# Optimization experiments

Measured on AMD Instinct MI355X. Metric: run time of the kernel, lower is better.

Reference implementation:

```python
import jax, jax.numpy as jnp
import numpy as np

B, N, K = 4, 8192, 16
EMBED, HID, NCLS = 64, 128, 13
EPS = 1e-5


def _bn(x, g, b):
    # BatchNorm1d in training mode: stats over all points (B*N), per channel
    m = jnp.mean(x, axis=(0, 1), keepdims=True)
    v = jnp.var(x, axis=(0, 1), keepdims=True)
    return (x - m) * jax.lax.rsqrt(v + EPS) * g + b


def _knn_idx(pos, k):
    # pos: [B,N,3] -> k nearest neighbor indices per point (self excluded)
    sq = jnp.sum(pos * pos, -1)  # [B,N]
    d2 = sq[:, :, None] + sq[:, None, :] - 2.0 * jnp.einsum('bnd,bmd->bnm', pos, pos)
    n = pos.shape[1]
    d2 = d2 + jnp.eye(n, dtype=pos.dtype) * 1e10  # mask self (loop=False)
    _, idx = jax.lax.top_k(-d2, k)  # [B,N,k]
    return idx


def _pt_conv(x, pos, idx, w_lin, w_src, w_dst, pos_w, pos_b):
    # PyG PointTransformerConv: vector attention over neighbors (incl. self loop)
    Bc = x.shape[0]
    bidx = jnp.arange(Bc)[:, None, None]
    v = x @ w_lin          # value:  lin(x)
    a_src = x @ w_src      # lin_src(x)
    a_dst = x @ w_dst      # lin_dst(x)
    vj = v[bidx, idx]                      # [B,N,k1,C]
    aj = a_src[bidx, idx]                  # [B,N,k1,C]
    pj = pos[bidx, idx]                    # [B,N,k1,3]
    delta = (pos[:, :, None, :] - pj) @ pos_w + pos_b   # pos_nn(pos_i - pos_j)
    attn = jax.nn.softmax(a_dst[:, :, None, :] - aj + delta, axis=2)
    return jnp.sum(attn * (vj + delta), axis=2)  # sum aggregation


def setup_inputs() -> dict:
    key = jax.random.key(0)
    ks = jax.random.split(key, 20)

    def w(k, fan_in, fan_out):
        return (jax.random.normal(k, (fan_in, fan_out), jnp.float32) / np.sqrt(fan_in)).astype(jnp.float32)

    inp = {
        'points': jax.random.normal(ks[0], (B, N, 3), jnp.float32),
        'embed_w1': w(ks[1], 3, EMBED), 'embed_b1': jnp.zeros((EMBED,), jnp.float32),
        'bn1_g': jnp.ones((EMBED,), jnp.float32), 'bn1_b': jnp.zeros((EMBED,), jnp.float32),
        'embed_w2': w(ks[2], EMBED, EMBED), 'embed_b2': jnp.zeros((EMBED,), jnp.float32),
        'bne_g': jnp.ones((EMBED,), jnp.float32), 'bne_b': jnp.zeros((EMBED,), jnp.float32),
        'l0_lin': w(ks[3], EMBED, HID), 'l0_src': w(ks[4], EMBED, HID), 'l0_dst': w(ks[5], EMBED, HID),
        'l0_pos_w': w(ks[6], 3, HID), 'l0_pos_b': jnp.zeros((HID,), jnp.float32),
        'l0_bn_g': jnp.ones((HID,), jnp.float32), 'l0_bn_b': jnp.zeros((HID,), jnp.float32),
        'l1_lin': w(ks[7], HID, HID), 'l1_src': w(ks[8], HID, HID), 'l1_dst': w(ks[9], HID, HID),
        'l1_pos_w': w(ks[10], 3, HID), 'l1_pos_b': jnp.zeros((HID,), jnp.float32),
        'l1_bn_g': jnp.ones((HID,), jnp.float32), 'l1_bn_b': jnp.zeros((HID,), jnp.float32),
        'dec_w1': w(ks[11], HID, HID), 'dec_b1': jnp.zeros((HID,), jnp.float32),
        'dec_bn_g': jnp.ones((HID,), jnp.float32), 'dec_bn_b': jnp.zeros((HID,), jnp.float32),
        'dec_w2': w(ks[12], HID, NCLS), 'dec_b2': jnp.zeros((NCLS,), jnp.float32),
    }
    return inp


def reference(points, embed_w1, embed_b1, bn1_g, bn1_b, embed_w2, embed_b2,
              bne_g, bne_b,
              l0_lin, l0_src, l0_dst, l0_pos_w, l0_pos_b, l0_bn_g, l0_bn_b,
              l1_lin, l1_src, l1_dst, l1_pos_w, l1_pos_b, l1_bn_g, l1_bn_b,
              dec_w1, dec_b1, dec_bn_g, dec_bn_b, dec_w2, dec_b2):
    Bc, Nc, _ = points.shape
    # embedding MLP: Linear -> BN -> ReLU -> Linear, then BN -> ReLU
    h = points @ embed_w1 + embed_b1
    h = jax.nn.relu(_bn(h, bn1_g, bn1_b))
    h = h @ embed_w2 + embed_b2
    x = jax.nn.relu(_bn(h, bne_g, bne_b))
    # kNN graph (per batch), then append self loop (add_self_loops=True)
    idx = _knn_idx(points, K)
    self_idx = jnp.broadcast_to(jnp.arange(Nc)[None, :, None], (Bc, Nc, 1))
    idxf = jnp.concatenate([idx, self_idx], axis=-1)  # [B,N,K+1]
    x = jax.nn.relu(_bn(_pt_conv(x, points, idxf, l0_lin, l0_src, l0_dst, l0_pos_w, l0_pos_b), l0_bn_g, l0_bn_b))
    x = jax.nn.relu(_bn(_pt_conv(x, points, idxf, l1_lin, l1_src, l1_dst, l1_pos_w, l1_pos_b), l1_bn_g, l1_bn_b))
    # decoder MLP (dropout = identity at inference)
    h = jax.nn.relu(_bn(x @ dec_w1 + dec_b1, dec_bn_g, dec_bn_b))
    logits = h @ dec_w2 + dec_b2  # [B,N,num_classes]
    return logits
```

## Files before the change

### kernel.cpp

```cpp
#include <hip/hip_runtime.h>
#include <math.h>

#define BB 4
#define NN 8192
#define PP 32768
#define KNN 16
#define KINF 3.4e38f
#define PADIDX 0x7fffffff

typedef float f32x2 __attribute__((ext_vector_type(2)));
typedef float f32x4 __attribute__((ext_vector_type(4)));

__device__ __forceinline__ f32x2 pk_mul(f32x2 a, f32x2 b) {
  f32x2 d; asm("v_pk_mul_f32 %0, %1, %2" : "=v"(d) : "v"(a), "v"(b)); return d;
}
__device__ __forceinline__ f32x2 pk_add(f32x2 a, f32x2 b) {
  f32x2 d; asm("v_pk_add_f32 %0, %1, %2" : "=v"(d) : "v"(a), "v"(b)); return d;
}

__global__ __launch_bounds__(256) void k_embed1(const float* __restrict__ pts,
    const float* __restrict__ w1, const float* __restrict__ b1, float* __restrict__ h1)
{
  int tid = threadIdx.x;
  int c = tid & 63, g = tid >> 6;
  float wx = w1[c], wy = w1[64 + c], wz = w1[128 + c], bc = b1[c];
  int base = blockIdx.x * 256;
  #pragma unroll 4
  for (int i = 0; i < 64; ++i) {
    int p = base + g + i * 4;
    float px = pts[p*3+0], py = pts[p*3+1], pz = pts[p*3+2];
    float h = fmaf(pz, wz, fmaf(py, wy, fmaf(px, wx, bc)));
    h1[(size_t)p*64 + c] = h;
  }
}

__global__ __launch_bounds__(256) void k_prep(const float* __restrict__ pts, float* __restrict__ pp)
{
  int t = blockIdx.x * 256 + threadIdx.x;
  int b = t >> 12, m = t & 4095;
  int c = m >> 4, l = m & 15;
  int jl = b * NN + c * 32 + l;
  int jh = jl + 16;
  float xl = pts[jl*3+0], yl = pts[jl*3+1], zl = pts[jl*3+2];
  float xh = pts[jh*3+0], yh = pts[jh*3+1], zh = pts[jh*3+2];
  float wl = __fadd_rn(__fadd_rn(__fmul_rn(xl,xl), __fmul_rn(yl,yl)), __fmul_rn(zl,zl));
  float wh = __fadd_rn(__fadd_rn(__fmul_rn(xh,xh), __fmul_rn(yh,yh)), __fmul_rn(zh,zh));
  float* o = pp + (size_t)t * 8;
  *(float4*)(o + 0) = make_float4(xl, xh, yl, yh);
  *(float4*)(o + 4) = make_float4(zl, zh, wl, wh);
}

template<int C>
__global__ __launch_bounds__(256) void k_stats(const float* __restrict__ src,
    float* __restrict__ gsum, float* __restrict__ gss)
{
  constexpr int GPB = 256 / C;
  int tid = threadIdx.x;
  int c = tid % C, g = tid / C;
  float s = 0.f, ss = 0.f;
  for (int p = blockIdx.x * GPB + g; p < PP; p += gridDim.x * GPB) {
    float v = src[(size_t)p*C + c];
    s += v; ss = fmaf(v, v, ss);
  }
  __shared__ float ls[256], lq[256];
  ls[tid] = s; lq[tid] = ss;
  __syncthreads();
  if (tid < C) {
    float a = 0.f, b2 = 0.f;
    #pragma unroll
    for (int i = 0; i < GPB; ++i) { a += ls[tid + i*C]; b2 += lq[tid + i*C]; }
    atomicAdd(gsum + tid, a);
    atomicAdd(gss + tid, b2);
  }
}

__global__ void k_finalize(int C, const float* __restrict__ gsum, const float* __restrict__ gss,
    const float* __restrict__ gg, const float* __restrict__ bb,
    float* __restrict__ sc, float* __restrict__ sh)
{
  int c = threadIdx.x;
  if (c >= C) return;
  float mean = gsum[c] * (1.0f / PP);
  float var  = gss[c] * (1.0f / PP) - mean * mean;
  float s = gg[c] / sqrtf(var + 1e-5f);
  sc[c] = s;
  sh[c] = bb[c] - mean * s;
}

template<int K, int COUT>
__global__ __launch_bounds__(256) void k_proj(const float* __restrict__ in,
    const float* __restrict__ sc, const float* __restrict__ sh,
    const float* __restrict__ W0, const float* __restrict__ W1, const float* __restrict__ W2,
    const float* __restrict__ B0, const float* __restrict__ B1, const float* __restrict__ B2,
    float* __restrict__ O0, float* __restrict__ O1, float* __restrict__ O2)
{
  constexpr int PTS = 64;
  constexpr int CW = 8;
  constexpr int CG = COUT / CW;
  constexpr int PW = PTS * CG / 256;
  const float* W  = (blockIdx.y == 0) ? W0 : (blockIdx.y == 1) ? W1 : W2;
  const float* Bb = (blockIdx.y == 0) ? B0 : (blockIdx.y == 1) ? B1 : B2;
  float*       O  = (blockIdx.y == 0) ? O0 : (blockIdx.y == 1) ? O1 : O2;
  __shared__ float xs[PTS][K + 1];
  int tid = threadIdx.x;
  int pbase = blockIdx.x * PTS;
  constexpr int T4 = PTS * K / 4;
  for (int i = tid; i < T4; i += 256) {
    int p = i / (K/4), k = (i % (K/4)) * 4;
    float4 v = *(const float4*)(in + (size_t)(pbase + p)*K + k);
    v.x = fmaxf(fmaf(v.x, sc[k+0], sh[k+0]), 0.f);
    v.y = fmaxf(fmaf(v.y, sc[k+1], sh[k+1]), 0.f);
    v.z = fmaxf(fmaf(v.z, sc[k+2], sh[k+2]), 0.f);
    v.w = fmaxf(fmaf(v.w, sc[k+3], sh[k+3]), 0.f);
    xs[p][k+0] = v.x; xs[p][k+1] = v.y; xs[p][k+2] = v.z; xs[p][k+3] = v.w;
  }
  __syncthreads();
  int cg = tid % CG, pg = tid / CG;
  int c0 = cg * CW, p0 = pg * PW;
  float acc[PW][CW];
  #pragma unroll
  for (int i = 0; i < PW; ++i) {
    #pragma unroll
    for (int j = 0; j < CW; ++j) acc[i][j] = 0.f;
  }
  #pragma unroll 4
  for (int k = 0; k < K; ++k) {
    float4 wa = *(const float4*)(W + (size_t)k*COUT + c0);
    float4 wb = *(const float4*)(W + (size_t)k*COUT + c0 + 4);
    #pragma unroll
    for (int i = 0; i < PW; ++i) {
      float x = xs[p0 + i][k];
      acc[i][0] = fmaf(x, wa.x, acc[i][0]);
      acc[i][1] = fmaf(x, wa.y, acc[i][1]);
      acc[i][2] = fmaf(x, wa.z, acc[i][2]);
      acc[i][3] = fmaf(x, wa.w, acc[i][3]);
      acc[i][4] = fmaf(x, wb.x, acc[i][4]);
      acc[i][5] = fmaf(x, wb.y, acc[i][5]);
      acc[i][6] = fmaf(x, wb.z, acc[i][6]);
      acc[i][7] = fmaf(x, wb.w, acc[i][7]);
    }
  }
  float bj[CW];
  #pragma unroll
  for (int j = 0; j < CW; ++j) bj[j] = Bb ? Bb[c0 + j] : 0.f;
  #pragma unroll
  for (int i = 0; i < PW; ++i) {
    float* op = O + (size_t)(pbase + p0 + i)*COUT + c0;
    *(float4*)(op)     = make_float4(acc[i][0]+bj[0], acc[i][1]+bj[1], acc[i][2]+bj[2], acc[i][3]+bj[3]);
    *(float4*)(op + 4) = make_float4(acc[i][4]+bj[4], acc[i][5]+bj[5], acc[i][6]+bj[6], acc[i][7]+bj[7]);
  }
}

__global__ __launch_bounds__(256, 8) void k_knn(const float* __restrict__ pp, int* __restrict__ idxout)
{
  __shared__ uint2 buf[256];
  int tid = threadIdx.x;
  int lane = tid & 63;
  int l16 = lane & 15;
  int g64 = lane & 48;
  uint2* wbuf = buf + (tid >> 6) * 64;
  int wv = (blockIdx.x * 256 + tid) >> 6;
  int b  = wv >> 11;
  int qbase = (wv * 4) & (NN - 1);
  int qc = qbase >> 5;
  int qr = (qbase & 31) + (lane >> 4);
  const float* pb = pp + (size_t)b * (NN * 4);

  float qx, qy, qz, qw;
  {
    int qslot = qc * 16 + (qr & 15);
    int qh = (qr >> 4) & 1;
    const float* qp = pb + (size_t)qslot * 8 + qh;
    qx = qp[0]; qy = qp[2]; qz = qp[4]; qw = qp[6];
  }
  f32x2 qx2; qx2.x = qx; qx2.y = qx;
  f32x2 qy2; qy2.x = qy; qy2.y = qy;
  f32x2 qz2; qz2.x = qz; qz2.y = qz;
  f32x2 qw2; qw2.x = qw; qw2.y = qw;

  float lval = KINF; int lidx = PADIDX;
  float pval = KINF; int pidx = PADIDX;
  int   pcnt = 0;
  float tau  = KINF;
  unsigned lmask = (1u << l16) - 1;

  auto flush = [&]() {
    float v = (l16 >= pcnt) ? KINF : pval;
    int  ix = (l16 >= pcnt) ? PADIDX : pidx;
    #pragma unroll
    for (int k = 2; k <= 16; k <<= 1) {
      #pragma unroll
      for (int m = k >> 1; m >= 1; m >>= 1) {
        float ov = __shfl_xor(v, m, 16);
        int   oi = __shfl_xor(ix, m, 16);
        bool dirUp = (l16 & k) == 0;
        bool lower = (l16 & m) == 0;
        bool oLt = (ov < v) || (ov == v && oi < ix);
        if ((dirUp == lower) ? oLt : !oLt) { v = ov; ix = oi; }
      }
    }
    float rv = __shfl_xor(v, 15, 16);
    int   ri = __shfl_xor(ix, 15, 16);
    bool t = (rv < lval) || (rv == lval && ri < lidx);
    float nv = t ? rv : lval;
    int   ni = t ? ri : lidx;
    #pragma unroll
    for (int m = 8; m >= 1; m >>= 1) {
      float ov = __shfl_xor(nv, m, 16);
      int   oi = __shfl_xor(ni, m, 16);
      bool lower = (l16 & m) == 0;
      bool oLt = (ov < nv) || (ov == nv && oi < ni);
      if (lower ? oLt : !oLt) { nv = ov; ni = oi; }
    }
    lval = nv; lidx = ni;
    tau = __shfl(lval, 15, 16);
    pcnt = 0;
  };

  auto append = [&](unsigned long long bal, bool hit, float d2, int j) {
    unsigned slice = (unsigned)(bal >> g64) & 0xffffu;
    int h   = __popc(slice);
    int pos = __popc(slice & lmask);
    if (__ballot(pcnt + h > 16)) flush();
    if (hit) wbuf[g64 + pcnt + pos] = make_uint2(__float_as_uint(d2), (unsigned)j);
    uint2 r = wbuf[lane];
    bool targ = (l16 >= pcnt) && (l16 < pcnt + h);
    pval = targ ? __uint_as_float(r.x) : pval;
    pidx = targ ? (int)r.y : pidx;
    pcnt += h;
  };

  const float* cp = pb + (size_t)l16 * 8;
  for (int c = 0; c < 256; ++c) {
    f32x4 A  = *(const f32x4*)(cp + 0);
    f32x4 Bq = *(const f32x4*)(cp + 4);
    cp += 128;
    f32x2 xs = __builtin_shufflevector(A, A, 0, 1);
    f32x2 ys = __builtin_shufflevector(A, A, 2, 3);
    f32x2 zs = __builtin_shufflevector(Bq, Bq, 0, 1);
    f32x2 ws = __builtin_shufflevector(Bq, Bq, 2, 3);
    f32x2 dot = pk_add(pk_add(pk_mul(qx2, xs), pk_mul(qy2, ys)), pk_mul(qz2, zs));
    f32x2 s2  = pk_add(qw2, ws);
    f32x2 t2  = pk_add(dot, dot);
    float d2lo = __fsub_rn(s2.x, t2.x);
    float d2hi = __fsub_rn(s2.y, t2.y);
    if (c == qc) {
      bool lo = qr < 16;
      int  tl = lo ? qr : qr - 16;
      if (l16 == tl) { if (lo) d2lo = KINF; else d2hi = KINF; }
    }
    bool hlo = d2lo < tau;
    unsigned long long blo = __ballot(hlo);
    if (blo) append(blo, hlo, d2lo, c * 32 + l16);
    bool hhi = d2hi < tau;
    unsigned long long bhi = __ballot(hhi);
    if (bhi) append(bhi, hhi, d2hi, c * 32 + 16 + l16);
  }
  flush();

  idxout[(size_t)wv * 64 + lane] = lidx;
}

__global__ __launch_bounds__(256) void k_conv(const float* __restrict__ V, const float* __restrict__ S,
    const float* __restrict__ D, const float* __restrict__ pts, const int* __restrict__ idx,
    const float* __restrict__ pw, const float* __restrict__ pbv, float* __restrict__ Y)
{
  int lane = threadIdx.x & 63;
  int wid  = (blockIdx.x * 256 + threadIdx.x) >> 6;
  int c0 = lane * 2;
  float2 w0  = *(const float2*)(pw + c0);
  float2 w1  = *(const float2*)(pw + 128 + c0);
  float2 w2  = *(const float2*)(pw + 256 + c0);
  float2 pb2 = *(const float2*)(pbv + c0);
  for (int p = wid; p < PP; p += 4096) {
    int b = p >> 13, self = p & (NN - 1);
    const float* pbase = pts + (size_t)b * NN * 3;
    float pix = pbase[self*3+0], piy = pbase[self*3+1], piz = pbase[self*3+2];
    float2 di = *(const float2*)(D + (size_t)p*128 + c0);
    float m0 = -3.4e38f, m1 = -3.4e38f, l0 = 0.f, l1 = 0.f, a0 = 0.f, a1 = 0.f;
    for (int t = 0; t < 17; ++t) {
      int j = (t < 16) ? idx[p*KNN + t] : self;
      float dx = pix - pbase[j*3+0];
      float dy = piy - pbase[j*3+1];
      float dz = piz - pbase[j*3+2];
      size_t off = ((size_t)b * NN + j) * 128 + c0;
      float2 sj = *(const float2*)(S + off);
      float2 vj = *(const float2*)(V + off);
      float de0 = fmaf(dz, w2.x, fmaf(dy, w1.x, fmaf(dx, w0.x, pb2.x)));
      float de1 = fmaf(dz, w2.y, fmaf(dy, w1.y, fmaf(dx, w0.y, pb2.y)));
      float g0 = di.x - sj.x + de0;
      float g1 = di.y - sj.y + de1;
      float mn0 = fmaxf(m0, g0), mn1 = fmaxf(m1, g1);
      float cr0 = __expf(m0 - mn0), cr1 = __expf(m1 - mn1);
      float e0  = __expf(g0 - mn0), e1  = __expf(g1 - mn1);
      l0 = fmaf(l0, cr0, e0);
      l1 = fmaf(l1, cr1, e1);
      a0 = fmaf(a0, cr0, e0 * (vj.x + de0));
      a1 = fmaf(a1, cr1, e1 * (vj.y + de1));
      m0 = mn0; m1 = mn1;
    }
    float2 o; o.x = a0 / l0; o.y = a1 / l1;
    *(float2*)(Y + (size_t)p*128 + c0) = o;
  }
}

__global__ __launch_bounds__(256) void k_dec2(const float* __restrict__ T,
    const float* __restrict__ sc, const float* __restrict__ sh,
    const float* __restrict__ W, const float* __restrict__ bias, float* __restrict__ out)
{
  __shared__ float xs[64][132];
  __shared__ float wt[13][128];
  int tid = threadIdx.x;
  int pb = blockIdx.x * 64;
  for (int i = tid; i < 13 * 128; i += 256) {
    int cls = i >> 7, k = i & 127;
    wt[cls][k] = W[k*13 + cls];
  }
  for (int i = tid; i < 64 * 32; i += 256) {
    int p = i >> 5, k = (i & 31) * 4;
    float4 v = *(const float4*)(T + (size_t)(pb + p)*128 + k);
    v.x = fmaxf(fmaf(v.x, sc[k+0], sh[k+0]), 0.f);
    v.y = fmaxf(fmaf(v.y, sc[k+1], sh[k+1]), 0.f);
    v.z = fmaxf(fmaf(v.z, sc[k+2], sh[k+2]), 0.f);
    v.w = fmaxf(fmaf(v.w, sc[k+3], sh[k+3]), 0.f);
    xs[p][k+0] = v.x; xs[p][k+1] = v.y; xs[p][k+2] = v.z; xs[p][k+3] = v.w;
  }
  __syncthreads();
  for (int o = tid; o < 64 * 13; o += 256) {
    int p = o / 13, cls = o - p * 13;
    float acc = bias[cls];
    const float4* xr = (const float4*)&xs[p][0];
    const float4* wr = (const float4*)&wt[cls][0];
    #pragma unroll 8
    for (int k4 = 0; k4 < 32; ++k4) {
      float4 a = xr[k4], w = wr[k4];
      acc = fmaf(a.x, w.x, acc);
      acc = fmaf(a.y, w.y, acc);
      acc = fmaf(a.z, w.z, acc);
      acc = fmaf(a.w, w.w, acc);
    }
    out[(size_t)(pb + p)*13 + cls] = acc;
  }
}

extern "C" void kernel_launch(void* const* d_in, const int* in_sizes, int n_in,
                              void* d_out, int out_size, void* d_ws, size_t ws_size,
                              hipStream_t stream)
{
  const float* pts      = (const float*)d_in[0];
  const float* embed_w1 = (const float*)d_in[1];
  const float* embed_b1 = (const float*)d_in[2];
  const float* bn1_g    = (const float*)d_in[3];
  const float* bn1_b    = (const float*)d_in[4];
  const float* embed_w2 = (const float*)d_in[5];
  const float* embed_b2 = (const float*)d_in[6];
  const float* bne_g    = (const float*)d_in[7];
  const float* bne_b    = (const float*)d_in[8];
  const float* l0_lin   = (const float*)d_in[9];
  const float* l0_src   = (const float*)d_in[10];
  const float* l0_dst   = (const float*)d_in[11];
  const float* l0_pos_w = (const float*)d_in[12];
  const float* l0_pos_b = (const float*)d_in[13];
  const float* l0_bn_g  = (const float*)d_in[14];
  const float* l0_bn_b  = (const float*)d_in[15];
  const float* l1_lin   = (const float*)d_in[16];
  const float* l1_src   = (const float*)d_in[17];
  const float* l1_dst   = (const float*)d_in[18];
  const float* l1_pos_w = (const float*)d_in[19];
  const float* l1_pos_b = (const float*)d_in[20];
  const float* l1_bn_g  = (const float*)d_in[21];
  const float* l1_bn_b  = (const float*)d_in[22];
  const float* dec_w1   = (const float*)d_in[23];
  const float* dec_b1   = (const float*)d_in[24];
  const float* dec_bn_g = (const float*)d_in[25];
  const float* dec_bn_b = (const float*)d_in[26];
  const float* dec_w2   = (const float*)d_in[27];
  const float* dec_b2   = (const float*)d_in[28];

  char* ws = (char*)d_ws;
  const size_t MB = 1024 * 1024;
  float* h1  = (float*)(ws + 0);
  float* h2  = (float*)(ws + 8*MB);
  int*   idx = (int*)  (ws + 16*MB);
  float* v0  = (float*)(ws + 18*MB);
  float* s0  = (float*)(ws + 34*MB);
  float* d0  = (float*)(ws + 50*MB);
  float* y0  = (float*)(ws + 66*MB);
  float* y1  = (float*)(ws + 82*MB);
  float* tt  = (float*)(ws + 0);
  float* pairs8 = (float*)(ws + 18*MB);
  float* st  = (float*)(ws + 98*MB);
  float *sum1=st+0,    *ss1=st+64,   *sc1=st+128,  *sh1=st+192;
  float *sum2=st+256,  *ss2=st+320,  *sc2=st+384,  *sh2=st+448;
  float *sum3=st+512,  *ss3=st+640,  *sc3=st+768,  *sh3=st+896;
  float *sum4=st+1024, *ss4=st+1152, *sc4=st+1280, *sh4=st+1408;
  float *sum5=st+1536, *ss5=st+1664, *sc5=st+1792, *sh5=st+1920;

  hipMemsetAsync(st, 0, 2048 * sizeof(float), stream);

  k_prep<<<64, 256, 0, stream>>>(pts, pairs8);
  k_knn<<<2048, 256, 0, stream>>>(pairs8, idx);

  k_embed1<<<128, 256, 0, stream>>>(pts, embed_w1, embed_b1, h1);
  k_stats<64><<<512, 256, 0, stream>>>(h1, sum1, ss1);
  k_finalize<<<1, 64, 0, stream>>>(64, sum1, ss1, bn1_g, bn1_b, sc1, sh1);
  k_proj<64,64><<<dim3(512,1), 256, 0, stream>>>(h1, sc1, sh1,
      embed_w2, embed_w2, embed_w2, embed_b2, embed_b2, embed_b2, h2, h2, h2);
  k_stats<64><<<512, 256, 0, stream>>>(h2, sum2, ss2);
  k_finalize<<<1, 64, 0, stream>>>(64, sum2, ss2, bne_g, bne_b, sc2, sh2);

  k_proj<64,128><<<dim3(512,3), 256, 0, stream>>>(h2, sc2, sh2,
      l0_lin, l0_src, l0_dst, nullptr, nullptr, nullptr, v0, s0, d0);
  k_conv<<<1024, 256, 0, stream>>>(v0, s0, d0, pts, idx, l0_pos_w, l0_pos_b, y0);
  k_stats<128><<<512, 256, 0, stream>>>(y0, sum3, ss3);
  k_finalize<<<1, 128, 0, stream>>>(128, sum3, ss3, l0_bn_g, l0_bn_b, sc3, sh3);

  k_proj<128,128><<<dim3(512,3), 256, 0, stream>>>(y0, sc3, sh3,
      l1_lin, l1_src, l1_dst, nullptr, nullptr, nullptr, v0, s0, d0);
  k_conv<<<1024, 256, 0, stream>>>(v0, s0, d0, pts, idx, l1_pos_w, l1_pos_b, y1);
  k_stats<128><<<512, 256, 0, stream>>>(y1, sum4, ss4);
  k_finalize<<<1, 128, 0, stream>>>(128, sum4, ss4, l1_bn_g, l1_bn_b, sc4, sh4);

  k_proj<128,128><<<dim3(512,1), 256, 0, stream>>>(y1, sc4, sh4,
      dec_w1, dec_w1, dec_w1, dec_b1, dec_b1, dec_b1, tt, tt, tt);
  k_stats<128><<<512, 256, 0, stream>>>(tt, sum5, ss5);
  k_finalize<<<1, 128, 0, stream>>>(128, sum5, ss5, dec_bn_g, dec_bn_b, sc5, sh5);
  k_dec2<<<512, 256, 0, stream>>>(tt, sc5, sh5, dec_w2, dec_b2, (float*)d_out);
}
```

Baseline: 698.9 us.

## Process four query groups per wave in kNN to reuse candidate loads

Each wave in the kNN kernel now handles 16 queries (4 register-blocked groups of 4) instead of 4, so every candidate point loaded from memory is compared against four times as many queries. Candidate loads are software-prefetched one iteration ahead. The pending-buffer handling is simplified: flush now reads directly from LDS instead of maintaining a register copy on every append. The grid shrinks to 512 blocks and the occupancy hint is removed, trading parallelism and occupancy for higher register use and more per-wave work.

New measurement: 802.0 us. 1.15x slower.

```diff
diff --git a/kernel.cpp b/kernel.cpp
--- a/kernel.cpp
+++ b/kernel.cpp
@@ -151,42 +151,43 @@
   }
 }
 
-__global__ __launch_bounds__(256, 8) void k_knn(const float* __restrict__ pp, int* __restrict__ idxout)
-{
-  __shared__ uint2 buf[256];
+__global__ __launch_bounds__(256) void k_knn(const float* __restrict__ pp, int* __restrict__ idxout)
+{
+  __shared__ uint2 buf[4][4][64];
   int tid = threadIdx.x;
   int lane = tid & 63;
   int l16 = lane & 15;
+  int g   = lane >> 4;
   int g64 = lane & 48;
-  uint2* wbuf = buf + (tid >> 6) * 64;
-  int wv = (blockIdx.x * 256 + tid) >> 6;
-  int b  = wv >> 11;
-  int qbase = (wv * 4) & (NN - 1);
-  int qc = qbase >> 5;
-  int qr = (qbase & 31) + (lane >> 4);
+  int wid = tid >> 6;
+  int wv = blockIdx.x * 4 + wid;
+  int b  = wv >> 9;
+  int qbase = (wv & 511) << 4;
+  int qc    = qbase >> 5;
+  int qhalf = (qbase >> 4) & 1;
   const float* pb = pp + (size_t)b * (NN * 4);
 
-  float qx, qy, qz, qw;
-  {
-    int qslot = qc * 16 + (qr & 15);
-    int qh = (qr >> 4) & 1;
-    const float* qp = pb + (size_t)qslot * 8 + qh;
-    qx = qp[0]; qy = qp[2]; qz = qp[4]; qw = qp[6];
-  }
-  f32x2 qx2; qx2.x = qx; qx2.y = qx;
-  f32x2 qy2; qy2.x = qy; qy2.y = qy;
-  f32x2 qz2; qz2.x = qz; qz2.y = qz;
-  f32x2 qw2; qw2.x = qw; qw2.y = qw;
-
-  float lval = KINF; int lidx = PADIDX;
-  float pval = KINF; int pidx = PADIDX;
-  int   pcnt = 0;
-  float tau  = KINF;
+  f32x2 qx2[4], qy2[4], qz2[4], qw2[4];
+  #pragma unroll
+  for (int r = 0; r < 4; ++r) {
+    const float* qp = pb + (size_t)(qc * 16 + r * 4 + g) * 8 + qhalf;
+    float x = qp[0], y = qp[2], z = qp[4], w = qp[6];
+    qx2[r].x = x; qx2[r].y = x;
+    qy2[r].x = y; qy2[r].y = y;
+    qz2[r].x = z; qz2[r].y = z;
+    qw2[r].x = w; qw2[r].y = w;
+  }
+
+  float lval[4]; int lidx[4]; float tau[4]; int pcnt[4];
+  #pragma unroll
+  for (int r = 0; r < 4; ++r) { lval[r] = KINF; lidx[r] = PADIDX; tau[r] = KINF; pcnt[r] = 0; }
   unsigned lmask = (1u << l16) - 1;
-
-  auto flush = [&]() {
-    float v = (l16 >= pcnt) ? KINF : pval;
-    int  ix = (l16 >= pcnt) ? PADIDX : pidx;
+  int sdiff = l16 - g;
+
+  auto flush = [&](int r) {
+    uint2 e = buf[wid][r][lane];
+    float v  = (l16 < pcnt[r]) ? __uint_as_float(e.x) : KINF;
+    int  ix  = (l16 < pcnt[r]) ? (int)e.y : PADIDX;
     #pragma unroll
     for (int k = 2; k <= 16; k <<= 1) {
       #pragma unroll
@@ -201,9 +202,9 @@
     }
     float rv = __shfl_xor(v, 15, 16);
     int   ri = __shfl_xor(ix, 15, 16);
-    bool t = (rv < lval) || (rv == lval && ri < lidx);
-    float nv = t ? rv : lval;
-    int   ni = t ? ri : lidx;
+    bool t = (rv < lval[r]) || (rv == lval[r] && ri < lidx[r]);
+    float nv = t ? rv : lval[r];
+    int   ni = t ? ri : lidx[r];
     #pragma unroll
     for (int m = 8; m >= 1; m >>= 1) {
       float ov = __shfl_xor(nv, m, 16);
@@ -212,53 +213,59 @@
       bool oLt = (ov < nv) || (ov == nv && oi < ni);
       if (lower ? oLt : !oLt) { nv = ov; ni = oi; }
     }
-    lval = nv; lidx = ni;
-    tau = __shfl(lval, 15, 16);
-    pcnt = 0;
+    lval[r] = nv; lidx[r] = ni;
+    tau[r] = __shfl(nv, 15, 16);
+    pcnt[r] = 0;
   };
 
-  auto append = [&](unsigned long long bal, bool hit, float d2, int j) {
+  auto append = [&](int r, unsigned long long bal, bool hit, float d2, int j) {
     unsigned slice = (unsigned)(bal >> g64) & 0xffffu;
     int h   = __popc(slice);
     int pos = __popc(slice & lmask);
-    if (__ballot(pcnt + h > 16)) flush();
-    if (hit) wbuf[g64 + pcnt + pos] = make_uint2(__float_as_uint(d2), (unsigned)j);
-    uint2 r = wbuf[lane];
-    bool targ = (l16 >= pcnt) && (l16 < pcnt + h);
-    pval = targ ? __uint_as_float(r.x) : pval;
-    pidx = targ ? (int)r.y : pidx;
-    pcnt += h;
+    if (__ballot(pcnt[r] + h > 16)) flush(r);
+    if (hit) buf[wid][r][g64 + pcnt[r] + pos] = make_uint2(__float_as_uint(d2), (unsigned)j);
+    pcnt[r] += h;
   };
 
   const float* cp = pb + (size_t)l16 * 8;
+  f32x4 A  = *(const f32x4*)(cp + 0);
+  f32x4 Bq = *(const f32x4*)(cp + 4);
   for (int c = 0; c < 256; ++c) {
-    f32x4 A  = *(const f32x4*)(cp + 0);
-    f32x4 Bq = *(const f32x4*)(cp + 4);
     cp += 128;
+    f32x4 An = *(const f32x4*)(cp + 0);
+    f32x4 Bn = *(const f32x4*)(cp + 4);
     f32x2 xs = __builtin_shufflevector(A, A, 0, 1);
     f32x2 ys = __builtin_shufflevector(A, A, 2, 3);
     f32x2 zs = __builtin_shufflevector(Bq, Bq, 0, 1);
     f32x2 ws = __builtin_shufflevector(Bq, Bq, 2, 3);
-    f32x2 dot = pk_add(pk_add(pk_mul(qx2, xs), pk_mul(qy2, ys)), pk_mul(qz2, zs));
-    f32x2 s2  = pk_add(qw2, ws);
-    f32x2 t2  = pk_add(dot, dot);
-    float d2lo = __fsub_rn(s2.x, t2.x);
-    float d2hi = __fsub_rn(s2.y, t2.y);
-    if (c == qc) {
-      bool lo = qr < 16;
-      int  tl = lo ? qr : qr - 16;
-      if (l16 == tl) { if (lo) d2lo = KINF; else d2hi = KINF; }
-    }
-    bool hlo = d2lo < tau;
-    unsigned long long blo = __ballot(hlo);
-    if (blo) append(blo, hlo, d2lo, c * 32 + l16);
-    bool hhi = d2hi < tau;
-    unsigned long long bhi = __ballot(hhi);
-    if (bhi) append(bhi, hhi, d2hi, c * 32 + 16 + l16);
-  }
-  flush();
-
-  idxout[(size_t)wv * 64 + lane] = lidx;
+    bool atqc = (c == qc);
+    #pragma unroll
+    for (int r = 0; r < 4; ++r) {
+      f32x2 dot = pk_add(pk_add(pk_mul(qx2[r], xs), pk_mul(qy2[r], ys)), pk_mul(qz2[r], zs));
+      f32x2 s2  = pk_add(qw2[r], ws);
+      f32x2 t2  = pk_add(dot, dot);
+      float d2lo = __fsub_rn(s2.x, t2.x);
+      float d2hi = __fsub_rn(s2.y, t2.y);
+      if (atqc) {
+        bool self = (sdiff == r * 4);
+        if (qhalf == 0) { if (self) d2lo = KINF; }
+        else            { if (self) d2hi = KINF; }
+      }
+      bool hlo = d2lo < tau[r];
+      unsigned long long blo = __ballot(hlo);
+      if (blo) append(r, blo, hlo, d2lo, c * 32 + l16);
+      bool hhi = d2hi < tau[r];
+      unsigned long long bhi = __ballot(hhi);
+      if (bhi) append(r, bhi, hhi, d2hi, c * 32 + 16 + l16);
+    }
+    A = An; Bq = Bn;
+  }
+  #pragma unroll
+  for (int r = 0; r < 4; ++r) flush(r);
+
+  size_t base = ((size_t)(b * NN + qbase)) * 16;
+  #pragma unroll
+  for (int r = 0; r < 4; ++r) idxout[base + r * 64 + lane] = lidx[r];
 }
 
 __global__ __launch_bounds__(256) void k_conv(const float* __restrict__ V, const float* __restrict__ S,
@@ -399,7 +406,7 @@
   hipMemsetAsync(st, 0, 2048 * sizeof(float), stream);
 
   k_prep<<<64, 256, 0, stream>>>(pts, pairs8);
-  k_knn<<<2048, 256, 0, stream>>>(pairs8, idx);
+  k_knn<<<512, 256, 0, stream>>>(pairs8, idx);
 
   k_embed1<<<128, 256, 0, stream>>>(pts, embed_w1, embed_b1, h1);
   k_stats<64><<<512, 256, 0, stream>>>(h1, sum1, ss1);
```
